# Optimization experiments

Measured on AMD Instinct MI355X. Metric: run time of the kernel, lower is better.

Reference implementation:

```python
import jax, jax.numpy as jnp
import numpy as np

B, S, E, H = 2, 2048, 1024, 16
DH = E // H  # 64


def setup_inputs() -> dict:
    key = jax.random.key(0)
    ks = jax.random.split(key, 13)
    s = 1.0 / np.sqrt(E)
    inp = {
        'query': jax.random.normal(ks[0], (B, S, E), jnp.float32),
        'key':   jax.random.normal(ks[1], (B, S, E), jnp.float32),
        'value': jax.random.normal(ks[2], (B, S, E), jnp.float32),
        # nn.Linear weights stored [out, in]
        'Wq': jax.random.uniform(ks[3], (E, E), jnp.float32, -s, s),
        'bq': jax.random.uniform(ks[4], (E,), jnp.float32, -s, s),
        'Wk': jax.random.uniform(ks[5], (E, E), jnp.float32, -s, s),
        'bk': jax.random.uniform(ks[6], (E,), jnp.float32, -s, s),
        'Wv': jax.random.uniform(ks[7], (E, E), jnp.float32, -s, s),
        'bv': jax.random.uniform(ks[8], (E,), jnp.float32, -s, s),
        # 1x1 Conv2d over head channels: weight [H, H] (squeezed from [H,H,1,1]), bias [H]
        'Wc': jax.random.uniform(ks[9], (H, H), jnp.float32, -1.0 / np.sqrt(H), 1.0 / np.sqrt(H)),
        'bc': jax.random.uniform(ks[10], (H,), jnp.float32, -1.0 / np.sqrt(H), 1.0 / np.sqrt(H)),
        'Wo': jax.random.uniform(ks[11], (E, E), jnp.float32, -s, s),
        'bo': jax.random.uniform(ks[12], (E,), jnp.float32, -s, s),
    }
    return inp


def reference(query, key, value, Wq, bq, Wk, bk, Wv, bv, Wc, bc, Wo, bo):
    b, s = query.shape[0], query.shape[1]
    # projections -> (B, H, S, Dh)
    def split_heads(x):
        return x.reshape(b, s, H, DH).transpose(0, 2, 1, 3)
    Q = split_heads(query @ Wq.T + bq)
    K = split_heads(key @ Wk.T + bk)
    V = split_heads(value @ Wv.T + bv)
    # raw scores (B, H, S, S)
    scores = jnp.einsum('bhqd,bhkd->bhqk', Q, K) / np.sqrt(DH).astype(np.float32)
    # 1x1 conv mixes logits across heads: channel-wise matmul + bias
    noise = jnp.einsum('gh,bhqk->bgqk', Wc, scores) + bc[None, :, None, None]
    scores = scores + noise
    weights = jax.nn.softmax(scores, axis=-1)
    out = jnp.einsum('bhqk,bhkd->bhqd', weights, V)  # (B, H, S, Dh)
    out = out.transpose(0, 2, 1, 3).reshape(b, s, E)
    return out @ Wo.T + bo
```

## Files before the change

### kernel.cpp

```cpp
#include <hip/hip_runtime.h>


typedef __attribute__((ext_vector_type(8))) short bf16x8_t;
typedef __attribute__((ext_vector_type(4))) short bf16x4_t;
typedef __attribute__((ext_vector_type(4))) float f32x4_t;

__device__ inline unsigned short f2bf(float f) {
  unsigned u = __builtin_bit_cast(unsigned, f);
  u += 0x7fffu + ((u >> 16) & 1u);
  return (unsigned short)(u >> 16);
}

#define GLOAD(dst, ptr) \
  asm volatile("global_load_dwordx4 %0, %1, off" : "=v"(dst) : "v"((const void*)(ptr)))
#define WAITV0() { asm volatile("s_waitcnt vmcnt(0)"); __builtin_amdgcn_sched_barrier(0); }

__device__ inline void bar_lds() {
  asm volatile("s_waitcnt lgkmcnt(0)" ::: "memory");
  __builtin_amdgcn_s_barrier();
}

struct ConvArgs {
  const float* src[7];
  unsigned short* dst[7];
  int n[7];
};

__global__ __launch_bounds__(256) void convert_f32_bf16(ConvArgs a) {
  const int which = blockIdx.y;
  const int i = (blockIdx.x * 256 + threadIdx.x) * 8;
  if (i >= a.n[which]) return;
  const float* s = a.src[which] + i;
  f32x4_t x0 = *(const f32x4_t*)(s);
  f32x4_t x1 = *(const f32x4_t*)(s + 4);
  bf16x8_t o;
#pragma unroll
  for (int j = 0; j < 4; j++) o[j] = (short)f2bf(x0[j]);
#pragma unroll
  for (int j = 0; j < 4; j++) o[4 + j] = (short)f2bf(x1[j]);
  *(bf16x8_t*)(a.dst[which] + i) = o;
}

struct GemmArgs {
  const unsigned short* A[3];
  const unsigned short* Bt[3];
  const float* bias[3];
  void* C[3];
  int f32out[3];
};

__global__ __launch_bounds__(256) void gemm_bt(GemmArgs ga, int M, int N, int K)
{
  __shared__ unsigned short As[128 * 32];
  __shared__ unsigned short Bs[128 * 32];
  const int z = blockIdx.z;
  const unsigned short* __restrict__ A  = ga.A[z];
  const unsigned short* __restrict__ Bt = ga.Bt[z];
  const float* __restrict__ bias = ga.bias[z];
  void* __restrict__ C = ga.C[z];
  const int f32out = ga.f32out[z];

  const int t = threadIdx.x;
  const int l = t & 63;
  const int w = t >> 6;
  const int quad = l >> 4, n16 = l & 15;
  const int wm = (w & 1) * 64, wn = (w >> 1) * 64;
  const long m0 = (long)blockIdx.x * 128, n0 = (long)blockIdx.y * 128;

  f32x4_t acc[4][4] = {};

  const unsigned short* gA = A + (m0 + (t >> 2)) * (long)K + (t & 3) * 8;
  const unsigned short* gB = Bt + (n0 + (t >> 2)) * (long)K + (t & 3) * 8;
  const long rowskip = 64l * K;

  bf16x8_t ra0, ra1, rb0, rb1;
  GLOAD(ra0, gA);            GLOAD(ra1, gA + rowskip);
  GLOAD(rb0, gB);            GLOAD(rb1, gB + rowskip);
  WAITV0();

  for (int kt = 0; kt < K; kt += 32) {
    bar_lds();
    *(bf16x8_t*)&As[t * 8] = ra0;
    *(bf16x8_t*)&As[2048 + t * 8] = ra1;
    *(bf16x8_t*)&Bs[t * 8] = rb0;
    *(bf16x8_t*)&Bs[2048 + t * 8] = rb1;
    bar_lds();
    const long ktn = (kt + 32 < K) ? kt + 32 : 0;
    GLOAD(ra0, gA + ktn);      GLOAD(ra1, gA + ktn + rowskip);
    GLOAD(rb0, gB + ktn);      GLOAD(rb1, gB + ktn + rowskip);

    bf16x8_t af[4], bfr[4];
#pragma unroll
    for (int i = 0; i < 4; i++) {
      af[i]  = *(const bf16x8_t*)&As[(wm + i * 16 + n16) * 32 + quad * 8];
      bfr[i] = *(const bf16x8_t*)&Bs[(wn + i * 16 + n16) * 32 + quad * 8];
    }
#pragma unroll
    for (int mi = 0; mi < 4; mi++)
#pragma unroll
      for (int ni = 0; ni < 4; ni++)
        acc[mi][ni] = __builtin_amdgcn_mfma_f32_16x16x32_bf16(af[mi], bfr[ni], acc[mi][ni], 0, 0, 0);
    WAITV0();
  }

#pragma unroll
  for (int ni = 0; ni < 4; ni++) {
    const long n = n0 + wn + ni * 16 + n16;
    const float bv = bias[n];
#pragma unroll
    for (int mi = 0; mi < 4; mi++) {
#pragma unroll
      for (int r = 0; r < 4; r++) {
        const long m = m0 + wm + mi * 16 + quad * 4 + r;
        const float v = acc[mi][ni][r] + bv;
        if (f32out) ((float*)C)[m * N + n] = v;
        else ((unsigned short*)C)[m * N + n] = f2bf(v);
      }
    }
  }
}

__global__ __launch_bounds__(256) void transpose_v(
    const unsigned short* __restrict__ V, unsigned short* __restrict__ VT)
{
  __shared__ unsigned short tile[64][72];
  const int t = threadIdx.x;
  const int s0 = blockIdx.x * 64, h = blockIdx.y, b = blockIdx.z;
#pragma unroll
  for (int r = 0; r < 2; r++) {
    const int elem = r * 2048 + t * 8;
    const int s = elem >> 6, d = elem & 63;
    *(bf16x8_t*)&tile[s][d] =
        *(const bf16x8_t*)&V[(size_t)(b * 2048 + s0 + s) * 1024 + h * 64 + d];
  }
  __syncthreads();
#pragma unroll
  for (int r = 0; r < 2; r++) {
    const int elem = r * 2048 + t * 8;
    const int d = elem >> 6, sl = elem & 63;
    bf16x8_t o;
#pragma unroll
    for (int j = 0; j < 8; j++) o[j] = (short)tile[sl + j][d];
    *(bf16x8_t*)&VT[((size_t)(b * 16 + h) * 64 + d) * 2048 + s0 + sl] = o;
  }
}

__global__ __launch_bounds__(1024, 8) void attention_fused(
    const unsigned short* __restrict__ Qb, const unsigned short* __restrict__ Kb,
    const unsigned short* __restrict__ VT, const float* __restrict__ Wc,
    float* __restrict__ Op0, float* __restrict__ Op1, float* __restrict__ Ll)
{
  __shared__ unsigned short sraw[512 * 36];
  __shared__ unsigned short pbuf[16 * 580];
  __shared__ unsigned short mmat[256];

  const int t = threadIdx.x;
  const int g = t >> 6, l = t & 63;
  const int quad = l >> 4, n16 = l & 15;

  const int id = blockIdx.x;
  const int xcd = id & 7;
  const int b = xcd >> 2;
  const int kb = (xcd >> 1) & 1;
  const int qb = (xcd & 1) * 64 + (id >> 3);
  const int q0 = qb * 16;
  const int k0 = kb * 1024;

  for (int i = t; i < 512 * 36; i += 1024) sraw[i] = 0;
  if (t < 256) {
    const float v = ((((t >> 4) == (t & 15)) ? 1.0f : 0.0f) + Wc[t]) * 0.1803368801111204f;
    mmat[t] = f2bf(v);
  }
  __syncthreads();

  bf16x8_t mfrag;
  if (quad < 2) mfrag = *(const bf16x8_t*)&mmat[n16 * 16 + quad * 8];
  else { bf16x8_t z = {0, 0, 0, 0, 0, 0, 0, 0}; mfrag = z; }
  const int c7 = g >> 2;

  bf16x8_t qf[2];
#pragma unroll
  for (int dr = 0; dr < 2; dr++)
    qf[dr] = *(const bf16x8_t*)&Qb[(size_t)(b * 2048 + q0 + n16) * 1024 + g * 64 + dr * 32 + quad * 8];

  const int slot = g ^ (quad << 3);
  const unsigned short* kptr = Kb + (size_t)(b * 2048 + k0 + n16) * 1024 + g * 64 + quad * 8;
  const unsigned short* vptr = VT + ((size_t)(b * 16 + g) * 64 + n16) * 2048 + k0 + quad * 8;

  bf16x8_t kf[2][2], vf[4];
  auto load_kf = [&](int kt) {
#pragma unroll
    for (int kc = 0; kc < 2; kc++)
#pragma unroll
      for (int dr = 0; dr < 2; dr++)
        kf[kc][dr] = *(const bf16x8_t*)(kptr + (size_t)(kt + kc * 16) * 1024 + dr * 32);
  };
  auto load_vf = [&](int kt) {
#pragma unroll
    for (int dc = 0; dc < 4; dc++)
      vf[dc] = *(const bf16x8_t*)(vptr + (size_t)dc * 16 * 2048 + kt);
  };
  auto qk_stage = [&]() {
    f32x4_t sf[2] = {};
#pragma unroll
    for (int kc = 0; kc < 2; kc++)
#pragma unroll
      for (int dr = 0; dr < 2; dr++)
        sf[kc] = __builtin_amdgcn_mfma_f32_16x16x32_bf16(qf[dr], kf[kc][dr], sf[kc], 0, 0, 0);
#pragma unroll
    for (int kc = 0; kc < 2; kc++)
#pragma unroll
      for (int r = 0; r < 4; r++)
        sraw[((quad * 4 + r) * 32 + kc * 16 + n16) * 36 + slot] = f2bf(sf[kc][r]);
  };

  load_kf(0);
  qk_stage();

  f32x4_t o[4] = {};
  float l_run = 0.0f;

  for (int it = 0; it < 32; ++it) {
    const int kt = it * 32;
    __syncthreads();

    load_vf(kt);

    f32x4_t mixd[2];
#pragma unroll
    for (int c2 = 0; c2 < 2; c2++) {
      const int c = g * 2 + c2;
      const unsigned short* sp = &sraw[(c * 16 + n16) * 36 + ((quad ^ c7) << 3)];
      bf16x4_t lo = *(const bf16x4_t*)sp;
      bf16x4_t hi = *(const bf16x4_t*)(sp + 4);
      bf16x8_t aa = {lo[0], lo[1], lo[2], lo[3], hi[0], hi[1], hi[2], hi[3]};
      f32x4_t z = {};
      mixd[c2] = __builtin_amdgcn_mfma_f32_16x16x32_bf16(aa, mfrag, z, 0, 0, 0);
    }

    float p[2][4];
    float lsum = 0.0f;
#pragma unroll
    for (int c2 = 0; c2 < 2; c2++)
#pragma unroll
      for (int r = 0; r < 4; r++) {
        p[c2][r] = exp2f(mixd[c2][r]);
        lsum += p[c2][r];
      }
    l_run += lsum;

    const int pbase = n16 * 580 + g * 36 + quad * 4;
#pragma unroll
    for (int c2 = 0; c2 < 2; c2++)
#pragma unroll
      for (int rp = 0; rp < 2; rp++) {
        unsigned pk;
        asm("v_cvt_pk_bf16_f32 %0, %1, %2"
            : "=v"(pk) : "v"(p[c2][2 * rp]), "v"(p[c2][2 * rp + 1]));
        *(unsigned*)&pbuf[pbase + c2 * 16 + 2 * rp] = pk;
      }

    __syncthreads();

    {
      const unsigned short* pp = &pbuf[g * 580 + n16 * 36 + quad * 8];
      bf16x4_t plo = *(const bf16x4_t*)pp;
      bf16x4_t phi = *(const bf16x4_t*)(pp + 4);
      bf16x8_t pf = {plo[0], plo[1], plo[2], plo[3], phi[0], phi[1], phi[2], phi[3]};
#pragma unroll
      for (int dc = 0; dc < 4; dc++)
        o[dc] = __builtin_amdgcn_mfma_f32_16x16x32_bf16(pf, vf[dc], o[dc], 0, 0, 0);
    }

    if (it < 31) {
      load_kf(kt + 32);
      qk_stage();
    }
  }

  l_run += __shfl_xor(l_run, 16);
  l_run += __shfl_xor(l_run, 32);
  if (quad == 0)
    Ll[((size_t)(kb * 2 + b) * 16 + n16) * 2048 + q0 + g] = l_run;
  float* const ob = kb ? Op1 : Op0;
#pragma unroll
  for (int dc = 0; dc < 4; dc++)
#pragma unroll
    for (int r = 0; r < 4; r++)
      ob[((size_t)(b * 2048 + q0 + quad * 4 + r)) * 1024 + g * 64 + dc * 16 + n16] = o[dc][r];
}

__global__ __launch_bounds__(256) void merge_halves(
    const float* __restrict__ Op0, const float* __restrict__ Op1,
    const float* __restrict__ Ll, unsigned short* __restrict__ Obuf)
{
  const int i = blockIdx.x * 256 + threadIdx.x;
  const size_t e8 = (size_t)i * 8;
  const int e = (int)(e8 & 1023);
  const int q = (int)((e8 >> 10) & 2047);
  const int b = (int)(e8 >> 21);
  const int h = e >> 6;
  const size_t row = (size_t)b * 2048 + q;
  const size_t mi = ((size_t)b * 16 + h) * 2048 + q;
  const float s = 1.0f / (Ll[mi] + Ll[2 * 16 * 2048 + mi]);
  const float* pa = Op0 + row * 1024 + e;
  const float* pb = Op1 + row * 1024 + e;
  f32x4_t a0 = *(const f32x4_t*)pa, a1 = *(const f32x4_t*)(pa + 4);
  f32x4_t b0 = *(const f32x4_t*)pb, b1 = *(const f32x4_t*)(pb + 4);
  bf16x8_t o8;
#pragma unroll
  for (int j = 0; j < 4; j++) o8[j] = (short)f2bf((a0[j] + b0[j]) * s);
#pragma unroll
  for (int j = 0; j < 4; j++) o8[4 + j] = (short)f2bf((a1[j] + b1[j]) * s);
  *(bf16x8_t*)&Obuf[row * 1024 + e] = o8;
}

extern "C" void kernel_launch(void* const* d_in, const int* in_sizes, int n_in,
                              void* d_out, int out_size, void* d_ws, size_t ws_size,
                              hipStream_t stream) {
  const float* query = (const float*)d_in[0];
  const float* key   = (const float*)d_in[1];
  const float* value = (const float*)d_in[2];
  const float* Wq = (const float*)d_in[3];
  const float* bq = (const float*)d_in[4];
  const float* Wk = (const float*)d_in[5];
  const float* bk = (const float*)d_in[6];
  const float* Wv = (const float*)d_in[7];
  const float* bv = (const float*)d_in[8];
  const float* Wc = (const float*)d_in[9];
  const float* Wo = (const float*)d_in[11];
  const float* bo = (const float*)d_in[12];

  char* ws = (char*)d_ws;
  const size_t MB = 1024 * 1024;
  unsigned short* q_bf  = (unsigned short*)(ws);
  unsigned short* k_bf  = (unsigned short*)(ws + 8 * MB);
  unsigned short* v_bf  = (unsigned short*)(ws + 16 * MB);
  unsigned short* wq_bf = (unsigned short*)(ws + 24 * MB);
  unsigned short* wk_bf = (unsigned short*)(ws + 26 * MB);
  unsigned short* wv_bf = (unsigned short*)(ws + 28 * MB);
  unsigned short* wo_bf = (unsigned short*)(ws + 30 * MB);
  unsigned short* Qb    = (unsigned short*)(ws + 32 * MB);
  unsigned short* Kb    = (unsigned short*)(ws + 40 * MB);
  unsigned short* Vb    = (unsigned short*)(ws + 48 * MB);
  float* Op0 = (float*)(ws + 56 * MB);
  float* Ll  = (float*)(ws + 72 * MB);
  float* Op1 = (float*)d_out;
  unsigned short* VT   = k_bf;
  unsigned short* Obuf = q_bf;

  ConvArgs ca;
  ca.src[0] = query; ca.dst[0] = q_bf;  ca.n[0] = 2 * 2048 * 1024;
  ca.src[1] = key;   ca.dst[1] = k_bf;  ca.n[1] = 2 * 2048 * 1024;
  ca.src[2] = value; ca.dst[2] = v_bf;  ca.n[2] = 2 * 2048 * 1024;
  ca.src[3] = Wq;    ca.dst[3] = wq_bf; ca.n[3] = 1024 * 1024;
  ca.src[4] = Wk;    ca.dst[4] = wk_bf; ca.n[4] = 1024 * 1024;
  ca.src[5] = Wv;    ca.dst[5] = wv_bf; ca.n[5] = 1024 * 1024;
  ca.src[6] = Wo;    ca.dst[6] = wo_bf; ca.n[6] = 1024 * 1024;
  convert_f32_bf16<<<dim3(2048, 7), 256, 0, stream>>>(ca);

  GemmArgs g3;
  g3.A[0] = q_bf; g3.Bt[0] = wq_bf; g3.bias[0] = bq; g3.C[0] = Qb; g3.f32out[0] = 0;
  g3.A[1] = k_bf; g3.Bt[1] = wk_bf; g3.bias[1] = bk; g3.C[1] = Kb; g3.f32out[1] = 0;
  g3.A[2] = v_bf; g3.Bt[2] = wv_bf; g3.bias[2] = bv; g3.C[2] = Vb; g3.f32out[2] = 0;
  gemm_bt<<<dim3(32, 8, 3), 256, 0, stream>>>(g3, 4096, 1024, 1024);

  transpose_v<<<dim3(32, 16, 2), 256, 0, stream>>>(Vb, VT);

  attention_fused<<<dim3(512), 1024, 0, stream>>>(Qb, Kb, VT, Wc, Op0, Op1, Ll);

  merge_halves<<<dim3(2048), 256, 0, stream>>>(Op0, Op1, Ll, Obuf);

  GemmArgs g1;
  g1.A[0] = Obuf; g1.Bt[0] = wo_bf; g1.bias[0] = bo; g1.C[0] = d_out; g1.f32out[0] = 1;
  g1.A[1] = g1.A[0]; g1.Bt[1] = g1.Bt[0]; g1.bias[1] = g1.bias[0]; g1.C[1] = g1.C[0]; g1.f32out[1] = 1;
  g1.A[2] = g1.A[0]; g1.Bt[2] = g1.Bt[0]; g1.bias[2] = g1.bias[0]; g1.C[2] = g1.C[0]; g1.f32out[2] = 1;
  gemm_bt<<<dim3(32, 8, 1), 256, 0, stream>>>(g1, 4096, 1024, 1024);
}
```

Baseline: 505.4 us.

## Halve attention block to 512 threads with each wave handling two heads

The fused attention kernel now launches 8 waves per block instead of 16, and each wave processes two heads. It computes QK scores, the head-mix MFMAs, softmax numerators and PV accumulation for both heads. V fragments are now loaded right before their PV MFMAs instead of being prefetched at the top of the iteration. The aim is to cut barrier cost across a large workgroup and give each wave more independent MFMA work. The trade-off is higher register pressure and less latency hiding on the V loads.

```diff
diff --git a/kernel.cpp b/kernel.cpp
--- a/kernel.cpp
+++ b/kernel.cpp
@@ -145,7 +145,7 @@
   }
 }
 
-__global__ __launch_bounds__(1024, 8) void attention_fused(
+__global__ __launch_bounds__(512, 4) void attention_fused(
     const unsigned short* __restrict__ Qb, const unsigned short* __restrict__ Kb,
     const unsigned short* __restrict__ VT, const float* __restrict__ Wc,
     float* __restrict__ Op0, float* __restrict__ Op1, float* __restrict__ Ll)
@@ -155,8 +155,9 @@
   __shared__ unsigned short mmat[256];
 
   const int t = threadIdx.x;
-  const int g = t >> 6, l = t & 63;
+  const int w = t >> 6, l = t & 63;
   const int quad = l >> 4, n16 = l & 15;
+  const int h0 = 2 * w, h1 = 2 * w + 1;
 
   const int id = blockIdx.x;
   const int xcd = id & 7;
@@ -166,7 +167,7 @@
   const int q0 = qb * 16;
   const int k0 = kb * 1024;
 
-  for (int i = t; i < 512 * 36; i += 1024) sraw[i] = 0;
+  for (int i = t; i < 512 * 36; i += 512) sraw[i] = 0;
   if (t < 256) {
     const float v = ((((t >> 4) == (t & 15)) ? 1.0f : 0.0f) + Wc[t]) * 0.1803368801111204f;
     mmat[t] = f2bf(v);
@@ -176,31 +177,29 @@
   bf16x8_t mfrag;
   if (quad < 2) mfrag = *(const bf16x8_t*)&mmat[n16 * 16 + quad * 8];
   else { bf16x8_t z = {0, 0, 0, 0, 0, 0, 0, 0}; mfrag = z; }
-  const int c7 = g >> 2;
-
-  bf16x8_t qf[2];
-#pragma unroll
-  for (int dr = 0; dr < 2; dr++)
-    qf[dr] = *(const bf16x8_t*)&Qb[(size_t)(b * 2048 + q0 + n16) * 1024 + g * 64 + dr * 32 + quad * 8];
-
-  const int slot = g ^ (quad << 3);
-  const unsigned short* kptr = Kb + (size_t)(b * 2048 + k0 + n16) * 1024 + g * 64 + quad * 8;
-  const unsigned short* vptr = VT + ((size_t)(b * 16 + g) * 64 + n16) * 2048 + k0 + quad * 8;
-
-  bf16x8_t kf[2][2], vf[4];
-  auto load_kf = [&](int kt) {
+  const int c7 = w >> 1;
+
+  bf16x8_t qf0[2], qf1[2];
+#pragma unroll
+  for (int dr = 0; dr < 2; dr++) {
+    qf0[dr] = *(const bf16x8_t*)&Qb[(size_t)(b * 2048 + q0 + n16) * 1024 + h0 * 64 + dr * 32 + quad * 8];
+    qf1[dr] = *(const bf16x8_t*)&Qb[(size_t)(b * 2048 + q0 + n16) * 1024 + h1 * 64 + dr * 32 + quad * 8];
+  }
+
+  const int slot0 = h0 ^ (quad << 3);
+  const int slot1 = h1 ^ (quad << 3);
+  const unsigned short* kptr0 = Kb + (size_t)(b * 2048 + k0 + n16) * 1024 + h0 * 64 + quad * 8;
+  const unsigned short* kptr1 = Kb + (size_t)(b * 2048 + k0 + n16) * 1024 + h1 * 64 + quad * 8;
+  const unsigned short* vptr0 = VT + ((size_t)(b * 16 + h0) * 64 + n16) * 2048 + k0 + quad * 8;
+  const unsigned short* vptr1 = VT + ((size_t)(b * 16 + h1) * 64 + n16) * 2048 + k0 + quad * 8;
+
+  auto qk_head = [&](const unsigned short* kp, const bf16x8_t* qf, int slot, int kt) {
+    bf16x8_t kf[2][2];
 #pragma unroll
     for (int kc = 0; kc < 2; kc++)
 #pragma unroll
       for (int dr = 0; dr < 2; dr++)
-        kf[kc][dr] = *(const bf16x8_t*)(kptr + (size_t)(kt + kc * 16) * 1024 + dr * 32);
-  };
-  auto load_vf = [&](int kt) {
-#pragma unroll
-    for (int dc = 0; dc < 4; dc++)
-      vf[dc] = *(const bf16x8_t*)(vptr + (size_t)dc * 16 * 2048 + kt);
-  };
-  auto qk_stage = [&]() {
+        kf[kc][dr] = *(const bf16x8_t*)(kp + (size_t)(kt + kc * 16) * 1024 + dr * 32);
     f32x4_t sf[2] = {};
 #pragma unroll
     for (int kc = 0; kc < 2; kc++)
@@ -214,22 +213,20 @@
         sraw[((quad * 4 + r) * 32 + kc * 16 + n16) * 36 + slot] = f2bf(sf[kc][r]);
   };
 
-  load_kf(0);
-  qk_stage();
-
-  f32x4_t o[4] = {};
-  float l_run = 0.0f;
+  qk_head(kptr0, qf0, slot0, 0);
+  qk_head(kptr1, qf1, slot1, 0);
+
+  f32x4_t o0[4] = {}, o1[4] = {};
+  float l_run0 = 0.0f, l_run1 = 0.0f;
 
   for (int it = 0; it < 32; ++it) {
     const int kt = it * 32;
     __syncthreads();
 
-    load_vf(kt);
-
-    f32x4_t mixd[2];
-#pragma unroll
-    for (int c2 = 0; c2 < 2; c2++) {
-      const int c = g * 2 + c2;
+    f32x4_t mixd[4];
+#pragma unroll
+    for (int c2 = 0; c2 < 4; c2++) {
+      const int c = 4 * w + c2;
       const unsigned short* sp = &sraw[(c * 16 + n16) * 36 + ((quad ^ c7) << 3)];
       bf16x4_t lo = *(const bf16x4_t*)sp;
       bf16x4_t hi = *(const bf16x4_t*)(sp + 4);
@@ -238,56 +235,79 @@
       mixd[c2] = __builtin_amdgcn_mfma_f32_16x16x32_bf16(aa, mfrag, z, 0, 0, 0);
     }
 
-    float p[2][4];
-    float lsum = 0.0f;
-#pragma unroll
-    for (int c2 = 0; c2 < 2; c2++)
+    float p[4][4];
+#pragma unroll
+    for (int c2 = 0; c2 < 4; c2++) {
+      float ls = 0.0f;
 #pragma unroll
       for (int r = 0; r < 4; r++) {
         p[c2][r] = exp2f(mixd[c2][r]);
-        lsum += p[c2][r];
-      }
-    l_run += lsum;
-
-    const int pbase = n16 * 580 + g * 36 + quad * 4;
-#pragma unroll
-    for (int c2 = 0; c2 < 2; c2++)
+        ls += p[c2][r];
+      }
+      if (c2 < 2) l_run0 += ls; else l_run1 += ls;
+    }
+
+#pragma unroll
+    for (int c2 = 0; c2 < 4; c2++) {
+      const int pb_ = n16 * 580 + (2 * w + (c2 >> 1)) * 36 + (c2 & 1) * 16 + quad * 4;
 #pragma unroll
       for (int rp = 0; rp < 2; rp++) {
         unsigned pk;
         asm("v_cvt_pk_bf16_f32 %0, %1, %2"
             : "=v"(pk) : "v"(p[c2][2 * rp]), "v"(p[c2][2 * rp + 1]));
-        *(unsigned*)&pbuf[pbase + c2 * 16 + 2 * rp] = pk;
-      }
+        *(unsigned*)&pbuf[pb_ + 2 * rp] = pk;
+      }
+    }
 
     __syncthreads();
 
     {
-      const unsigned short* pp = &pbuf[g * 580 + n16 * 36 + quad * 8];
+      const unsigned short* pp = &pbuf[h0 * 580 + n16 * 36 + quad * 8];
       bf16x4_t plo = *(const bf16x4_t*)pp;
       bf16x4_t phi = *(const bf16x4_t*)(pp + 4);
       bf16x8_t pf = {plo[0], plo[1], plo[2], plo[3], phi[0], phi[1], phi[2], phi[3]};
 #pragma unroll
-      for (int dc = 0; dc < 4; dc++)
-        o[dc] = __builtin_amdgcn_mfma_f32_16x16x32_bf16(pf, vf[dc], o[dc], 0, 0, 0);
+      for (int dc = 0; dc < 4; dc++) {
+        bf16x8_t vfd = *(const bf16x8_t*)(vptr0 + (size_t)dc * 16 * 2048 + kt);
+        o0[dc] = __builtin_amdgcn_mfma_f32_16x16x32_bf16(pf, vfd, o0[dc], 0, 0, 0);
+      }
+    }
+    {
+      const unsigned short* pp = &pbuf[h1 * 580 + n16 * 36 + quad * 8];
+      bf16x4_t plo = *(const bf16x4_t*)pp;
+      bf16x4_t phi = *(const bf16x4_t*)(pp + 4);
+      bf16x8_t pf = {plo[0], plo[1], plo[2], plo[3], phi[0], phi[1], phi[2], phi[3]};
+#pragma unroll
+      for (int dc = 0; dc < 4; dc++) {
+        bf16x8_t vfd = *(const bf16x8_t*)(vptr1 + (size_t)dc * 16 * 2048 + kt);
+        o1[dc] = __builtin_amdgcn_mfma_f32_16x16x32_bf16(pf, vfd, o1[dc], 0, 0, 0);
+      }
     }
 
     if (it < 31) {
-      load_kf(kt + 32);
-      qk_stage();
-    }
-  }
-
-  l_run += __shfl_xor(l_run, 16);
-  l_run += __shfl_xor(l_run, 32);
-  if (quad == 0)
-    Ll[((size_t)(kb * 2 + b) * 16 + n16) * 2048 + q0 + g] = l_run;
+      qk_head(kptr0, qf0, slot0, kt + 32);
+      qk_head(kptr1, qf1, slot1, kt + 32);
+    }
+  }
+
+  l_run0 += __shfl_xor(l_run0, 16);
+  l_run0 += __shfl_xor(l_run0, 32);
+  l_run1 += __shfl_xor(l_run1, 16);
+  l_run1 += __shfl_xor(l_run1, 32);
+  if (quad == 0) {
+    const size_t lbase = ((size_t)(kb * 2 + b) * 16 + n16) * 2048 + q0;
+    Ll[lbase + 2 * w]     = l_run0;
+    Ll[lbase + 2 * w + 1] = l_run1;
+  }
   float* const ob = kb ? Op1 : Op0;
 #pragma unroll
   for (int dc = 0; dc < 4; dc++)
 #pragma unroll
-    for (int r = 0; r < 4; r++)
-      ob[((size_t)(b * 2048 + q0 + quad * 4 + r)) * 1024 + g * 64 + dc * 16 + n16] = o[dc][r];
+    for (int r = 0; r < 4; r++) {
+      const size_t row = (size_t)(b * 2048 + q0 + quad * 4 + r) * 1024;
+      ob[row + h0 * 64 + dc * 16 + n16] = o0[dc][r];
+      ob[row + h1 * 64 + dc * 16 + n16] = o1[dc][r];
+    }
 }
 
 __global__ __launch_bounds__(256) void merge_halves(
@@ -367,7 +387,7 @@
 
   transpose_v<<<dim3(32, 16, 2), 256, 0, stream>>>(Vb, VT);
 
-  attention_fused<<<dim3(512), 1024, 0, stream>>>(Qb, Kb, VT, Wc, Op0, Op1, Ll);
+  attention_fused<<<dim3(512), 512, 0, stream>>>(Qb, Kb, VT, Wc, Op0, Op1, Ll);
 
   merge_halves<<<dim3(2048), 256, 0, stream>>>(Op0, Op1, Ll, Obuf);
 
```

Result: faster. 442.3 us (-12.5%).
